# Kernel optimization log

Measured on AMD Instinct MI355X. Metric: run time of the kernel, lower is better.

## Reference

```python
import jax, jax.numpy as jnp
import numpy as np

B, CIN, COUT, WDIM, RES, K = 16, 512, 512, 512, 64, 3
LRELU_SLOPE = 0.2
ACT_GAIN = np.sqrt(2.0).astype(np.float32)  # def_gain for 'lrelu'


def setup_inputs() -> dict:
    key = jax.random.key(0)
    ks = jax.random.split(key, 7)
    return {
        "x": jax.random.normal(ks[0], (B, CIN, RES, RES), dtype=jnp.float32),
        "w": jax.random.normal(ks[1], (B, WDIM), dtype=jnp.float32),
        "weight": jax.random.normal(ks[2], (COUT, CIN, K, K), dtype=jnp.float32),
        "affine_w": jax.random.normal(ks[3], (CIN, WDIM), dtype=jnp.float32),
        "affine_b": jnp.ones((CIN,), dtype=jnp.float32),  # bias_init=1
        "bias": jnp.zeros((COUT,), dtype=jnp.float32),
        "noise_const": jax.random.normal(ks[4], (RES, RES), dtype=jnp.float32),
        "noise_strength": jnp.float32(0.1),
    }


def reference(x, w, weight, affine_w, affine_b, bias, noise_const, noise_strength):
    # affine: FullyConnectedLayer with weight_gain = 1/sqrt(w_dim)
    wg = jnp.float32(1.0 / np.sqrt(WDIM))
    styles = w @ (affine_w * wg).T + affine_b  # [B, CIN]

    # fused modulated conv2d (demodulate=True, fused_modconv=True, up=down=1)
    wm = weight[None] * styles[:, None, :, None, None]  # [B, COUT, CIN, K, K]
    dcoefs = jax.lax.rsqrt(jnp.sum(wm * wm, axis=(2, 3, 4)) + 1e-8)  # [B, COUT]
    wm = wm * dcoefs[:, :, None, None, None]

    # grouped conv trick: groups = batch
    xg = x.reshape(1, B * CIN, RES, RES)
    wgk = wm.reshape(B * COUT, CIN, K, K)
    pad = K // 2
    y = jax.lax.conv_general_dilated(
        xg, wgk, window_strides=(1, 1), padding=[(pad, pad), (pad, pad)],
        dimension_numbers=("NCHW", "OIHW", "NCHW"), feature_group_count=B,
    ).reshape(B, COUT, RES, RES)

    # const noise injection
    y = y + noise_const * noise_strength

    # bias_act: bias + leaky_relu + gain (conv_clamp=None, gain=1.0)
    y = jax.nn.leaky_relu(y + bias[None, :, None, None], LRELU_SLOPE) * ACT_GAIN
    return y
```

## Files before the change

### kernel.cpp

```cpp
#include <hip/hip_runtime.h>

#define BATCH 16
#define CIN 512
#define COUT 512
#define RES 64

typedef __attribute__((ext_vector_type(8))) short bf16x8;
typedef __attribute__((ext_vector_type(4))) float f32x4;

__device__ __align__(16) unsigned short g_zero[64];

static __device__ __forceinline__ unsigned short f2bf(float f) {
    unsigned int u = __float_as_uint(f);
    u += 0x7fffu + ((u >> 16) & 1u);
    return (unsigned short)(u >> 16);
}

static __device__ __forceinline__ void gload16(const void* g, void* l) {
    __builtin_amdgcn_global_load_lds(
        (const __attribute__((address_space(1))) void*)g,
        (__attribute__((address_space(3))) void*)l, 16, 0, 0);
}

__global__ void k_styles(const float* __restrict__ w, const float* __restrict__ aw,
                         const float* __restrict__ ab, float* __restrict__ styles) {
    int wid  = (blockIdx.x * blockDim.x + threadIdx.x) >> 6;
    int lane = threadIdx.x & 63;
    int b = wid >> 9, i = wid & 511;
    const float* wrow = w + b * 512;
    const float* arow = aw + (size_t)i * 512;
    float acc = 0.f;
    for (int k = lane; k < 512; k += 64) acc += wrow[k] * arow[k];
    for (int off = 32; off; off >>= 1) acc += __shfl_down(acc, off, 64);
    if (lane == 0) styles[wid] = acc * 0.04419417382415922f + ab[i];
}

__global__ void k_dcoefs(const float* __restrict__ weight, const float* __restrict__ styles,
                         float* __restrict__ dcoefs) {
    int wid  = (blockIdx.x * blockDim.x + threadIdx.x) >> 6;
    int lane = threadIdx.x & 63;
    int b = wid >> 9, o = wid & 511;
    const float* wrow = weight + (size_t)o * 4608;
    const float* srow = styles + b * 512;
    float acc = 0.f;
    for (int i = lane; i < 512; i += 64) {
        float s = srow[i];
        float ss = 0.f;
#pragma unroll
        for (int k = 0; k < 9; ++k) { float v = wrow[i * 9 + k]; ss += v * v; }
        acc += s * s * ss;
    }
    for (int off = 32; off; off >>= 1) acc += __shfl_down(acc, off, 64);
    if (lane == 0) dcoefs[wid] = rsqrtf(acc + 1e-8f);
}

__global__ void k_wA(const float* __restrict__ weight, unsigned short* __restrict__ wA) {
    int o = blockIdx.x;
    __shared__ float lw[4608];
    for (int idx = threadIdx.x; idx < 4608; idx += 256)
        lw[idx] = weight[(size_t)o * 4608 + idx];
    __syncthreads();
    int i = threadIdx.x * 2;
#pragma unroll
    for (int t = 0; t < 9; ++t) {
        unsigned* dst = (unsigned*)(wA + (((size_t)t * COUT + o) << 9));
        dst[threadIdx.x] = (unsigned)f2bf(lw[i * 9 + t]) |
                           ((unsigned)f2bf(lw[(i + 1) * 9 + t]) << 16);
    }
}

__global__ void k_xpose(const float* __restrict__ x, const float* __restrict__ styles,
                        unsigned short* __restrict__ xt) {
    int bh = blockIdx.x;
    int ic = blockIdx.y;
    int b = bh >> 6, h = bh & 63;
    __shared__ float tile[32][65];
    __shared__ float st[32];
    const float* src = x + ((size_t)b * 512 + ic * 32) * 4096 + h * 64;
    if (threadIdx.x < 32) st[threadIdx.x] = styles[b * 512 + ic * 32 + threadIdx.x];
    for (int idx = threadIdx.x; idx < 2048; idx += 256) {
        int c = idx >> 6, w = idx & 63;
        tile[c][w] = src[(size_t)c * 4096 + w];
    }
    __syncthreads();
    int w = threadIdx.x >> 2, cg = (threadIdx.x & 3) * 8;
    bf16x8 v;
#pragma unroll
    for (int j = 0; j < 8; ++j) v[j] = (short)f2bf(tile[cg + j][w] * st[cg + j]);
    *(bf16x8*)(xt + (((size_t)bh * 64 + w) << 9) + ic * 32 + cg) = v;
}

__global__ __launch_bounds__(256, 2)
void k_conv(const unsigned short* __restrict__ wA, const unsigned short* __restrict__ xt,
            const float* __restrict__ dcoefs,
            const float* __restrict__ noise, const float* __restrict__ nstr,
            const float* __restrict__ bias, float* __restrict__ out) {
    __shared__ __align__(16) unsigned short lA[128 * 32];
    __shared__ __align__(16) unsigned short lB[128 * 32];
    const int tid = threadIdx.x;
    const int lane = tid & 63;
    const int wave = tid >> 6;
    const int b  = blockIdx.z;
    const int o0 = blockIdx.x * 128;
    const int p0 = blockIdx.y * 128;
    const int h0 = p0 >> 6;

    const unsigned short* gA0 = wA + ((size_t)(o0 + wave * 32 + (lane >> 2))) * 512
                                   + (lane & 3) * 8;
    const unsigned short* gA1 = gA0 + 16 * 512;
    void* ldsA0 = (void*)(lA + wave * 1024);
    void* ldsA1 = (void*)(lA + wave * 1024 + 512);
    void* ldsB0 = (void*)(lB + wave * 1024);
    void* ldsB1 = (void*)(lB + wave * 1024 + 512);

    const int fm_row = (wave >> 1) * 64 + (lane & 15);
    const int fn_row = (wave & 1) * 64 + (lane & 15);
    const int kof = (lane >> 4) * 8;

    f32x4 acc[4][4];
#pragma unroll
    for (int i = 0; i < 4; ++i)
#pragma unroll
        for (int j = 0; j < 4; ++j) acc[i][j] = (f32x4){0.f, 0.f, 0.f, 0.f};

    for (int t = 0; t < 9; ++t) {
        const int dy = t / 3 - 1, dx = t % 3 - 1;
        const unsigned short* gB[2];
        int adv[2];
#pragma unroll
        for (int s = 0; s < 2; ++s) {
            int pp = wave * 32 + s * 16 + (lane >> 2);
            int r = pp >> 6, w = pp & 63;
            int h = h0 + r + dy, ww = w + dx;
            bool valid = ((unsigned)h < 64u) && ((unsigned)ww < 64u);
            gB[s] = valid ? xt + (((size_t)b * 64 + h) * 64 + ww) * 512 + (lane & 3) * 8
                          : g_zero + (lane & 3) * 8;
            adv[s] = valid ? 32 : 0;
        }
        for (int i0 = 0; i0 < 16; ++i0) {
            __syncthreads();
            gload16(gA0, ldsA0);
            gload16(gA1, ldsA1);
            gload16(gB[0], ldsB0);
            gload16(gB[1], ldsB1);
            gA0 += 32; gA1 += 32; gB[0] += adv[0]; gB[1] += adv[1];
            asm volatile("s_waitcnt vmcnt(0)" ::: "memory");
            __syncthreads();

            bf16x8 af[4], bfr[4];
#pragma unroll
            for (int f = 0; f < 4; ++f)
                af[f] = *(const bf16x8*)&lA[(fm_row + f * 16) * 32 + kof];
#pragma unroll
            for (int f = 0; f < 4; ++f)
                bfr[f] = *(const bf16x8*)&lB[(fn_row + f * 16) * 32 + kof];
#pragma unroll
            for (int fm = 0; fm < 4; ++fm)
#pragma unroll
                for (int fn = 0; fn < 4; ++fn)
                    acc[fm][fn] = __builtin_amdgcn_mfma_f32_16x16x32_bf16(
                        af[fm], bfr[fn], acc[fm][fn], 0, 0, 0);
        }
        gA0 += 261632; gA1 += 261632;
    }

    const float ns = nstr[0];
    const float* dcb = dcoefs + b * 512;
#pragma unroll
    for (int fm = 0; fm < 4; ++fm) {
        int ob = o0 + (wave >> 1) * 64 + fm * 16 + (lane >> 4) * 4;
#pragma unroll
        for (int fn = 0; fn < 4; ++fn) {
            int p = p0 + (wave & 1) * 64 + fn * 16 + (lane & 15);
            float nval = noise[p] * ns;
#pragma unroll
            for (int rg = 0; rg < 4; ++rg) {
                int o = ob + rg;
                float v = acc[fm][fn][rg] * dcb[o] + nval + bias[o];
                v = (v > 0.f ? v : 0.2f * v) * 1.41421356f;
                out[((size_t)(b * COUT + o) << 12) + p] = v;
            }
        }
    }
}

__global__ void k_conv_naive(const float* __restrict__ x, const float* __restrict__ w,
                             const float* __restrict__ weight,
                             const float* __restrict__ aw, const float* __restrict__ ab,
                             const float* __restrict__ noise, const float* __restrict__ nstr,
                             const float* __restrict__ bias, float* __restrict__ out) {
    const int o = blockIdx.x, b = blockIdx.y;
    __shared__ float ss[512];
    __shared__ float red[256];
    const float* wv = w + b * 512;
    for (int i = threadIdx.x; i < 512; i += 256) {
        const float* arow = aw + (size_t)i * 512;
        float acc = 0.f;
        for (int k = 0; k < 512; ++k) acc += wv[k] * arow[k];
        ss[i] = acc * 0.04419417382415922f + ab[i];
    }
    __syncthreads();
    float part = 0.f;
    for (int i = threadIdx.x; i < 512; i += 256) {
        float s = ss[i], sq = 0.f;
#pragma unroll
        for (int k = 0; k < 9; ++k) { float v = weight[((size_t)o * 512 + i) * 9 + k]; sq += v * v; }
        part += s * s * sq;
    }
    red[threadIdx.x] = part;
    __syncthreads();
    for (int st = 128; st; st >>= 1) {
        if (threadIdx.x < st) red[threadIdx.x] += red[threadIdx.x + st];
        __syncthreads();
    }
    const float dcoef = rsqrtf(red[0] + 1e-8f);

    float acc[16];
#pragma unroll
    for (int j = 0; j < 16; ++j) acc[j] = 0.f;
    for (int i = 0; i < 512; ++i) {
        const float s = ss[i];
        float wk[9];
#pragma unroll
        for (int k = 0; k < 9; ++k) wk[k] = weight[((size_t)o * 512 + i) * 9 + k] * s;
        const float* xp = x + ((size_t)b * 512 + i) * 4096;
#pragma unroll
        for (int j = 0; j < 16; ++j) {
            const int p = (j << 8) + threadIdx.x;
            const int h = p >> 6, ww = p & 63;
            float a = acc[j];
#pragma unroll
            for (int ky = 0; ky < 3; ++ky) {
                int hh = h + ky - 1;
                if ((unsigned)hh < 64u) {
#pragma unroll
                    for (int kx = 0; kx < 3; ++kx) {
                        int wv2 = ww + kx - 1;
                        if ((unsigned)wv2 < 64u) a += wk[ky * 3 + kx] * xp[hh * 64 + wv2];
                    }
                }
            }
            acc[j] = a;
        }
    }
    const float ns = nstr[0], bs = bias[o];
#pragma unroll
    for (int j = 0; j < 16; ++j) {
        int p = (j << 8) + threadIdx.x;
        float v = acc[j] * dcoef + noise[p] * ns + bs;
        v = (v > 0.f ? v : 0.2f * v) * 1.41421356f;
        out[((size_t)(b * COUT + o) << 12) + p] = v;
    }
}

extern "C" void kernel_launch(void* const* d_in, const int* in_sizes, int n_in,
                              void* d_out, int out_size, void* d_ws, size_t ws_size,
                              hipStream_t stream) {
    const float* x   = (const float*)d_in[0];
    const float* w   = (const float*)d_in[1];
    const float* wt  = (const float*)d_in[2];
    const float* aw  = (const float*)d_in[3];
    const float* ab  = (const float*)d_in[4];
    const float* bs  = (const float*)d_in[5];
    const float* nc  = (const float*)d_in[6];
    const float* nst = (const float*)d_in[7];
    float* out = (float*)d_out;

    char* ws = (char*)d_ws;
    float* styles = (float*)ws;
    float* dcoefs = (float*)(ws + 32 * 1024);
    unsigned short* wA = (unsigned short*)(ws + (1 << 20));
    unsigned short* xt = (unsigned short*)(ws + (1 << 20) + 4718592ull);
    const size_t need = (size_t)(1 << 20) + 4718592ull + 67108864ull;

    if (d_ws != nullptr && ws_size >= need) {
        k_styles<<<2048, 256, 0, stream>>>(w, aw, ab, styles);
        k_dcoefs<<<2048, 256, 0, stream>>>(wt, styles, dcoefs);
        k_wA<<<512, 256, 0, stream>>>(wt, wA);
        k_xpose<<<dim3(1024, 16), 256, 0, stream>>>(x, styles, xt);
        k_conv<<<dim3(4, 32, 16), 256, 0, stream>>>(wA, xt, dcoefs, nc, nst, bs, out);
    } else {
        k_conv_naive<<<dim3(512, 16), 256, 0, stream>>>(x, w, wt, aw, ab, nc, nst, bs, out);
    }
}
```

Baseline: 636.3 us.

## Swizzle LDS k-chunks, remap conv blocks per XCD, fuse prep kernels

Applies an XOR swizzle to the 16-byte k-chunks staged in LDS so fragment reads avoid bank conflicts. Linearizes the conv grid and maps blocks so that all output-channel tiles of a pixel tile land on the same XCD, to improve L2 reuse of activations. Merges the styles and bf16 weight-conversion kernels and precomputes per-input-channel squared weight sums for the demodulation coefficients. Also vectorizes the activation transpose loads with float4.

```diff
diff --git a/kernel.cpp b/kernel.cpp
--- a/kernel.cpp
+++ b/kernel.cpp
@@ -22,51 +22,53 @@
         (__attribute__((address_space(3))) void*)l, 16, 0, 0);
 }
 
-__global__ void k_styles(const float* __restrict__ w, const float* __restrict__ aw,
-                         const float* __restrict__ ab, float* __restrict__ styles) {
-    int wid  = (blockIdx.x * blockDim.x + threadIdx.x) >> 6;
-    int lane = threadIdx.x & 63;
-    int b = wid >> 9, i = wid & 511;
-    const float* wrow = w + b * 512;
-    const float* arow = aw + (size_t)i * 512;
-    float acc = 0.f;
-    for (int k = lane; k < 512; k += 64) acc += wrow[k] * arow[k];
-    for (int off = 32; off; off >>= 1) acc += __shfl_down(acc, off, 64);
-    if (lane == 0) styles[wid] = acc * 0.04419417382415922f + ab[i];
-}
-
-__global__ void k_dcoefs(const float* __restrict__ weight, const float* __restrict__ styles,
+__global__ void k_prep1(const float* __restrict__ w, const float* __restrict__ aw,
+                        const float* __restrict__ ab, const float* __restrict__ weight,
+                        float* __restrict__ styles, unsigned short* __restrict__ wA,
+                        float* __restrict__ wsq) {
+    if (blockIdx.x < 2048) {
+        int wid  = (blockIdx.x * blockDim.x + threadIdx.x) >> 6;
+        int lane = threadIdx.x & 63;
+        int b = wid >> 9, i = wid & 511;
+        const float* wrow = w + b * 512;
+        const float* arow = aw + (size_t)i * 512;
+        float acc = 0.f;
+        for (int k = lane; k < 512; k += 64) acc += wrow[k] * arow[k];
+        for (int off = 32; off; off >>= 1) acc += __shfl_down(acc, off, 64);
+        if (lane == 0) styles[wid] = acc * 0.04419417382415922f + ab[i];
+    } else {
+        int o = blockIdx.x - 2048;
+        __shared__ float lw[4608];
+        for (int idx = threadIdx.x; idx < 4608; idx += 256)
+            lw[idx] = weight[(size_t)o * 4608 + idx];
+        __syncthreads();
+        int i = threadIdx.x * 2;
+        float sq0 = 0.f, sq1 = 0.f;
+#pragma unroll
+        for (int t = 0; t < 9; ++t) {
+            float v0 = lw[i * 9 + t], v1 = lw[(i + 1) * 9 + t];
+            sq0 += v0 * v0; sq1 += v1 * v1;
+            unsigned* dst = (unsigned*)(wA + (((size_t)t * COUT + o) << 9));
+            dst[threadIdx.x] = (unsigned)f2bf(v0) | ((unsigned)f2bf(v1) << 16);
+        }
+        *(float2*)(wsq + ((size_t)o << 9) + i) = make_float2(sq0, sq1);
+    }
+}
+
+__global__ void k_dcoefs(const float* __restrict__ wsq, const float* __restrict__ styles,
                          float* __restrict__ dcoefs) {
     int wid  = (blockIdx.x * blockDim.x + threadIdx.x) >> 6;
     int lane = threadIdx.x & 63;
     int b = wid >> 9, o = wid & 511;
-    const float* wrow = weight + (size_t)o * 4608;
     const float* srow = styles + b * 512;
+    const float* qrow = wsq + ((size_t)o << 9);
     float acc = 0.f;
     for (int i = lane; i < 512; i += 64) {
         float s = srow[i];
-        float ss = 0.f;
-#pragma unroll
-        for (int k = 0; k < 9; ++k) { float v = wrow[i * 9 + k]; ss += v * v; }
-        acc += s * s * ss;
+        acc += s * s * qrow[i];
     }
     for (int off = 32; off; off >>= 1) acc += __shfl_down(acc, off, 64);
     if (lane == 0) dcoefs[wid] = rsqrtf(acc + 1e-8f);
-}
-
-__global__ void k_wA(const float* __restrict__ weight, unsigned short* __restrict__ wA) {
-    int o = blockIdx.x;
-    __shared__ float lw[4608];
-    for (int idx = threadIdx.x; idx < 4608; idx += 256)
-        lw[idx] = weight[(size_t)o * 4608 + idx];
-    __syncthreads();
-    int i = threadIdx.x * 2;
-#pragma unroll
-    for (int t = 0; t < 9; ++t) {
-        unsigned* dst = (unsigned*)(wA + (((size_t)t * COUT + o) << 9));
-        dst[threadIdx.x] = (unsigned)f2bf(lw[i * 9 + t]) |
-                           ((unsigned)f2bf(lw[(i + 1) * 9 + t]) << 16);
-    }
 }
 
 __global__ void k_xpose(const float* __restrict__ x, const float* __restrict__ styles,
@@ -78,9 +80,10 @@
     __shared__ float st[32];
     const float* src = x + ((size_t)b * 512 + ic * 32) * 4096 + h * 64;
     if (threadIdx.x < 32) st[threadIdx.x] = styles[b * 512 + ic * 32 + threadIdx.x];
-    for (int idx = threadIdx.x; idx < 2048; idx += 256) {
-        int c = idx >> 6, w = idx & 63;
-        tile[c][w] = src[(size_t)c * 4096 + w];
+    for (int idx = threadIdx.x; idx < 512; idx += 256) {
+        int c = idx >> 4, w4 = (idx & 15) * 4;
+        float4 v = *(const float4*)(src + (size_t)c * 4096 + w4);
+        tile[c][w4] = v.x; tile[c][w4 + 1] = v.y; tile[c][w4 + 2] = v.z; tile[c][w4 + 3] = v.w;
     }
     __syncthreads();
     int w = threadIdx.x >> 2, cg = (threadIdx.x & 3) * 8;
@@ -100,13 +103,19 @@
     const int tid = threadIdx.x;
     const int lane = tid & 63;
     const int wave = tid >> 6;
-    const int b  = blockIdx.z;
-    const int o0 = blockIdx.x * 128;
-    const int p0 = blockIdx.y * 128;
+
+    const int lid = blockIdx.x;
+    const int xcd = lid & 7, grp = lid >> 3;
+    const int o_blk = grp & 3;
+    const int pair = ((grp >> 2) << 3) | xcd;
+    const int b = pair >> 5;
+    const int o0 = o_blk * 128;
+    const int p0 = (pair & 31) * 128;
     const int h0 = p0 >> 6;
 
-    const unsigned short* gA0 = wA + ((size_t)(o0 + wave * 32 + (lane >> 2))) * 512
-                                   + (lane & 3) * 8;
+    const int kqs = (lane & 3) ^ ((lane >> 3) & 3);
+
+    const unsigned short* gA0 = wA + ((size_t)(o0 + wave * 32 + (lane >> 2))) * 512 + kqs * 8;
     const unsigned short* gA1 = gA0 + 16 * 512;
     void* ldsA0 = (void*)(lA + wave * 1024);
     void* ldsA1 = (void*)(lA + wave * 1024 + 512);
@@ -115,7 +124,7 @@
 
     const int fm_row = (wave >> 1) * 64 + (lane & 15);
     const int fn_row = (wave & 1) * 64 + (lane & 15);
-    const int kof = (lane >> 4) * 8;
+    const int kof = (((lane >> 4) ^ ((lane >> 1) & 3)) & 3) * 8;
 
     f32x4 acc[4][4];
 #pragma unroll
@@ -133,8 +142,8 @@
             int r = pp >> 6, w = pp & 63;
             int h = h0 + r + dy, ww = w + dx;
             bool valid = ((unsigned)h < 64u) && ((unsigned)ww < 64u);
-            gB[s] = valid ? xt + (((size_t)b * 64 + h) * 64 + ww) * 512 + (lane & 3) * 8
-                          : g_zero + (lane & 3) * 8;
+            gB[s] = valid ? xt + (((size_t)b * 64 + h) * 64 + ww) * 512 + kqs * 8
+                          : g_zero + kqs * 8;
             adv[s] = valid ? 32 : 0;
         }
         for (int i0 = 0; i0 < 16; ++i0) {
@@ -269,16 +278,16 @@
     char* ws = (char*)d_ws;
     float* styles = (float*)ws;
     float* dcoefs = (float*)(ws + 32 * 1024);
-    unsigned short* wA = (unsigned short*)(ws + (1 << 20));
-    unsigned short* xt = (unsigned short*)(ws + (1 << 20) + 4718592ull);
-    const size_t need = (size_t)(1 << 20) + 4718592ull + 67108864ull;
+    float* wsq    = (float*)(ws + 64 * 1024);
+    unsigned short* wA = (unsigned short*)(ws + (2 << 20));
+    unsigned short* xt = (unsigned short*)(ws + (2 << 20) + 4718592ull);
+    const size_t need = (size_t)(2 << 20) + 4718592ull + 67108864ull;
 
     if (d_ws != nullptr && ws_size >= need) {
-        k_styles<<<2048, 256, 0, stream>>>(w, aw, ab, styles);
-        k_dcoefs<<<2048, 256, 0, stream>>>(wt, styles, dcoefs);
-        k_wA<<<512, 256, 0, stream>>>(wt, wA);
+        k_prep1<<<2560, 256, 0, stream>>>(w, aw, ab, wt, styles, wA, wsq);
+        k_dcoefs<<<2048, 256, 0, stream>>>(wsq, styles, dcoefs);
         k_xpose<<<dim3(1024, 16), 256, 0, stream>>>(x, styles, xt);
-        k_conv<<<dim3(4, 32, 16), 256, 0, stream>>>(wA, xt, dcoefs, nc, nst, bs, out);
+        k_conv<<<2048, 256, 0, stream>>>(wA, xt, dcoefs, nc, nst, bs, out);
     } else {
         k_conv_naive<<<dim3(512, 16), 256, 0, stream>>>(x, w, wt, aw, ab, nc, nst, bs, out);
     }
```

Measured after the change: 600.6 us. 5.6% less time.
